# Optimization experiments

Hardware: AMD Instinct MI355X
Metric: run time of the kernel (lower is better)

## Reference

```python
import jax, jax.numpy as jnp
import numpy as np

N_EMB = 8192
EMB_DIM = 128
BETA = 0.25


def setup_inputs() -> dict:
    key = jax.random.key(0)
    k1, k2 = jax.random.split(key)
    x = jax.random.normal(k1, (32, EMB_DIM, 1024), dtype=jnp.float32)
    embeddings = jax.random.normal(k2, (N_EMB, EMB_DIM), dtype=jnp.float32)
    return {"x": x, "embeddings": embeddings}


def reference(x, embeddings):
    # preprocess: swap chn_dim(=1) with last dim, flatten to tokens
    xt = jnp.swapaxes(x, 1, -1)                      # [B, L, D]
    flat = xt.reshape(-1, EMB_DIM)                   # [N, D]
    prenorm = jnp.linalg.norm(flat - jnp.mean(flat)) / np.sqrt(float(flat.size))

    # squared-euclidean distances via matmul + norms: [N, n_emb]
    s1 = jnp.sum(flat * flat, axis=1, keepdims=True)
    s2 = jnp.sum(embeddings * embeddings, axis=1)
    sim = flat @ embeddings.T
    distances = s1 + s2 - 2.0 * sim

    min_distance = jnp.min(distances, axis=1)
    idx = jnp.argmin(distances, axis=1)              # [N] int
    fit = jnp.mean(jnp.nan_to_num(min_distance))

    # EMA scatter statistics (one-hot matmul in torch == segment_sum here)
    k_sum = jax.ops.segment_sum(flat, idx, num_segments=N_EMB)         # [n_emb, D]
    k_elem = jax.ops.segment_sum(jnp.ones_like(idx, jnp.float32), idx,
                                 num_segments=N_EMB)                   # [n_emb]
    k_prob = k_elem / jnp.sum(k_elem)
    entropy = -jnp.sum(k_prob * jnp.log(k_prob + 1e-8))

    # embedding gather, reshape back to channels-first
    quantized = embeddings[idx].reshape(xt.shape)    # [B, L, D]
    quantized = jnp.swapaxes(quantized, 1, -1)       # [B, D, L]

    # ema_update=True -> codebook_loss = 0, only commit loss
    commit_loss = BETA * jnp.mean((jax.lax.stop_gradient(quantized) - x) ** 2)
    loss = commit_loss

    # straight-through estimator
    out = x + jax.lax.stop_gradient(quantized - x)
    return out, quantized, loss, fit, prenorm, entropy, k_sum, k_elem
```

## Files before the change

### kernel.cpp

```cpp
#include <hip/hip_runtime.h>
#include <math.h>
#include <float.h>

#define BB 32
#define DD 128
#define LL 1024
#define NN 32768
#define NE 8192
#define XSZ 4194304
#define OUT_OFF_Q     4194304
#define OUT_OFF_SCAL  8388608
#define OUT_OFF_KSUM  8388612
#define OUT_OFF_KELEM 9437188

typedef unsigned int u32;
typedef unsigned short u16;
typedef int   i32x4 __attribute__((ext_vector_type(4)));
typedef float f32x4 __attribute__((ext_vector_type(4)));

__device__ inline float waveSum(float v){
  #pragma unroll
  for (int o = 32; o > 0; o >>= 1) v += __shfl_down(v, o, 64);
  return v;
}
__device__ inline double waveSumD(double v){
  #pragma unroll
  for (int o = 32; o > 0; o >>= 1) v += __shfl_down(v, o, 64);
  return v;
}

__global__ __launch_bounds__(256) void prep_kernel(const float* __restrict__ e,
    u16* __restrict__ eh8, int* __restrict__ s2seed, float* __restrict__ s2f,
    int* __restrict__ cnt, float* __restrict__ accs)
{
  int t = threadIdx.x;
  if (blockIdx.x < 32) cnt[blockIdx.x * 256 + t] = 0;
  if (blockIdx.x == 32 && t < 16) accs[t] = 0.f;

  int row = blockIdx.x * 4 + (t >> 6);
  int kd  = t & 63;
  float2 ev = *reinterpret_cast<const float2*>(&e[row * DD + kd * 2]);
  int e0 = __float2int_rn(ev.x * 4096.f);
  int e1 = __float2int_rn(ev.y * 4096.f);
  e0 = min(max(e0, -32639), 32639);
  e1 = min(max(e1, -32639), 32639);
  double sq = (double)e0 * (double)e0 + (double)e1 * (double)e1;
  sq = waveSumD(sq);
  float sqf = ev.x * ev.x + ev.y * ev.y;
  sqf = waveSum(sqf);
  if (kd == 0){
    int sd = (int)(sq * (1.0 / 131072.0));
    sd = min(sd, 120000);
    s2seed[row] = -sd;
    s2f[row] = sqf;
  }
  int h0 = (e0 + 128) >> 8;
  int h1 = (e1 + 128) >> 8;
  int k = kd * 2;
  int T16 = row >> 4, lr = row & 15;
  int kt2 = k >> 6, lg = (k >> 4) & 3, j = k & 15;
  int du16 = (((T16*2 + kt2) * 1024) + lg*256 + lr*16 + j) >> 1;
  eh8[du16] = (u16)((h0 & 255) | ((h1 & 255) << 8));
}

#define LOADSET(AH0,AH1,SEED,TT) \
  { int T_ = (TT); \
    AH0 = *(const i32x4*)(ehp + (size_t)(T_*2 + 0) * 256); \
    AH1 = *(const i32x4*)(ehp + (size_t)(T_*2 + 1) * 256); \
    SEED = s2s4[T_*4 + sofs]; }

#define MFMA2S(SLOT, CT, AH0,AH1,SEED) \
  SLOT = __builtin_amdgcn_mfma_i32_16x16x64_i8(AH0, Bh[CT][0], SEED, 0,0,0); \
  SLOT = __builtin_amdgcn_mfma_i32_16x16x64_i8(AH1, Bh[CT][1], SLOT, 0,0,0);

#define KEYS1(T1V, CT, JV) \
  { _Pragma("unroll") \
    for (int r = 0; r < 4; ++r){ \
      int key = (int)(((u32)T1V[r] << 13) + (u32)(JV[r])); \
      int k2n; \
      asm("v_med3_i32 %0, %1, %2, %3" \
          : "=v"(k2n) : "v"(key), "v"(k1[CT]), "v"(k2[CT])); \
      k2[CT] = k2n; \
      k1[CT] = max(key, k1[CT]); \
    } }

#define TILE_BODY(AH0,AH1,SEED,JV) \
  MFMA2S(sa, 0, AH0,AH1,SEED) \
  MFMA2S(sb, 1, AH0,AH1,SEED) \
  KEYS1(sa, 0, JV) \
  MFMA2S(sa, 2, AH0,AH1,SEED) \
  KEYS1(sb, 1, JV) \
  MFMA2S(sb, 3, AH0,AH1,SEED) \
  KEYS1(sa, 2, JV) \
  KEYS1(sb, 3, JV)

__global__ __launch_bounds__(256, 4) void argmin_mfma(
    const float* __restrict__ x,
    const u32* __restrict__ eh8,
    const i32x4* __restrict__ s2s4,
    int* __restrict__ idx1o, int* __restrict__ idx2o)
{
  __shared__ int kk1[1024];
  __shared__ int kk2[1024];

  int t  = threadIdx.x;
  int w  = t >> 6;
  int l  = t & 63;
  int lr = l & 15;
  int lg = l >> 4;

  int blk  = blockIdx.x;
  int half = blk >> 9;
  int tb   = blk & 511;
  int hb64 = half * 64;

  int n0 = tb * 64;
  int b  = n0 >> 10;
  int l0 = n0 & 1023;
  const float* xb = x + (size_t)b * (DD * LL);

  i32x4 Bh[4][2];
  #pragma unroll
  for (int ct = 0; ct < 4; ++ct){
    int tok = l0 + ct*16 + lr;
    #pragma unroll
    for (int kt = 0; kt < 2; ++kt){
      #pragma unroll
      for (int dw = 0; dw < 4; ++dw){
        u32 hw = 0;
        #pragma unroll
        for (int bb = 0; bb < 4; ++bb){
          int k = kt*64 + lg*16 + dw*4 + bb;
          int xi = __float2int_rn(xb[(size_t)k * LL + tok] * 4096.f);
          xi = min(max(xi, -32639), 32639);
          int h  = (xi + 128) >> 8;
          hw |= ((u32)h & 255u) << (8*bb);
        }
        Bh[ct][kt][dw] = (int)hw;
      }
    }
  }

  int k1[4], k2[4];
  #pragma unroll
  for (int ct = 0; ct < 4; ++ct){ k1[ct] = (int)0x80000000; k2[ct] = (int)0x80000000; }

  int jvA[4], jvB[4];
  #pragma unroll
  for (int r = 0; r < 4; ++r){
    jvA[r] = 8191 - (hb64*64 + w*16 + lg*4 + r);
    jvB[r] = jvA[r] - 64;
  }

  const u32* ehp = eh8 + (size_t)l * 4;
  int sofs = lg;

  i32x4 Ah0A, Ah1A, seedA;
  i32x4 Ah0B, Ah1B, seedB;
  i32x4 sa, sb;

  LOADSET(Ah0A, Ah1A, seedA, (hb64 + 0)*4 + w)
  LOADSET(Ah0B, Ah1B, seedB, (hb64 + 1)*4 + w)

  for (int it = 0; it < 64; it += 2){
    TILE_BODY(Ah0A, Ah1A, seedA, jvA)
    if (it + 2 < 64){
      LOADSET(Ah0A, Ah1A, seedA, (hb64 + it + 2)*4 + w)
    }
    #pragma unroll
    for (int r = 0; r < 4; ++r) jvA[r] -= 128;

    TILE_BODY(Ah0B, Ah1B, seedB, jvB)
    if (it + 3 < 64){
      LOADSET(Ah0B, Ah1B, seedB, (hb64 + it + 3)*4 + w)
    }
    #pragma unroll
    for (int r = 0; r < 4; ++r) jvB[r] -= 128;
  }

  #pragma unroll
  for (int ct = 0; ct < 4; ++ct){
    int sidx = (ct*16 + lr)*16 + w*4 + lg;
    kk1[sidx] = k1[ct];
    kk2[sidx] = k2[ct];
  }
  __syncthreads();
  if (t < 64){
    int K1 = (int)0x80000000, K2 = (int)0x80000000;
    #pragma unroll 4
    for (int s = 0; s < 16; ++s){
      int a = kk1[t*16 + s], b2 = kk2[t*16 + s];
      int mn = min(a, K1);  K2 = max(mn, K2);  K1 = max(a, K1);
      mn = min(b2, K1);     K2 = max(mn, K2);  K1 = max(b2, K1);
    }
    idx1o[half*NN + n0 + t] = 8191 - (K1 & 8191);
    idx2o[half*NN + n0 + t] = 8191 - (K2 & 8191);
  }
}

__global__ __launch_bounds__(256) void fixup_kernel(const float* __restrict__ x,
    const float* __restrict__ e, const float* __restrict__ s2f,
    const int* __restrict__ idx1, const int* __restrict__ idx2,
    int* __restrict__ idxf, int* __restrict__ cnt, float* __restrict__ accs,
    float* __restrict__ out, float* __restrict__ quant, float* __restrict__ xT)
{
  __shared__ float red[5][4][64];
  __shared__ int jws[64];

  int t = threadIdx.x;
  int w = t >> 6, l = t & 63;
  int n0 = blockIdx.x * 64;
  int n  = n0 + l;
  int b  = n0 >> 10;
  int l0 = n0 & 1023;
  size_t base = (size_t)b * (DD * LL) + l0 + l;
  const float* xb = x + base;

  int js[4];
  js[0] = idx1[n];      js[1] = idx2[n];
  js[2] = idx1[NN + n]; js[3] = idx2[NN + n];

  float s1 = 0.f, sx = 0.f;
  float dt0 = 0.f, dt1 = 0.f, dt2 = 0.f, dt3 = 0.f;
  int kbase = w * 32;
  #pragma unroll
  for (int k4 = 0; k4 < 8; ++k4){
    int k = kbase + k4*4;
    float x0 = xb[(size_t)(k+0) * LL];
    float x1 = xb[(size_t)(k+1) * LL];
    float x2 = xb[(size_t)(k+2) * LL];
    float x3 = xb[(size_t)(k+3) * LL];
    s1 = fmaf(x0,x0, fmaf(x1,x1, fmaf(x2,x2, fmaf(x3,x3, s1))));
    sx += x0 + x1 + x2 + x3;
    if (xT) *(float4*)&xT[(size_t)n * DD + k] = make_float4(x0,x1,x2,x3);
    float4 v0 = *(const float4*)&e[(size_t)js[0] * DD + k];
    float4 v1 = *(const float4*)&e[(size_t)js[1] * DD + k];
    float4 v2 = *(const float4*)&e[(size_t)js[2] * DD + k];
    float4 v3 = *(const float4*)&e[(size_t)js[3] * DD + k];
    dt0 = fmaf(x0,v0.x, fmaf(x1,v0.y, fmaf(x2,v0.z, fmaf(x3,v0.w, dt0))));
    dt1 = fmaf(x0,v1.x, fmaf(x1,v1.y, fmaf(x2,v1.z, fmaf(x3,v1.w, dt1))));
    dt2 = fmaf(x0,v2.x, fmaf(x1,v2.y, fmaf(x2,v2.z, fmaf(x3,v2.w, dt2))));
    dt3 = fmaf(x0,v3.x, fmaf(x1,v3.y, fmaf(x2,v3.z, fmaf(x3,v3.w, dt3))));
  }
  red[0][w][l] = s1;
  red[1][w][l] = dt0;  red[2][w][l] = dt1;
  red[3][w][l] = dt2;  red[4][w][l] = dt3;
  sx = waveSum(sx);
  if (l == 0) atomicAdd(&accs[0], sx);
  __syncthreads();

  if (w == 0){
    float S1 = red[0][0][l] + red[0][1][l] + red[0][2][l] + red[0][3][l];
    float D[4];
    #pragma unroll
    for (int i = 0; i < 4; ++i)
      D[i] = red[1+i][0][l] + red[1+i][1][l] + red[1+i][2][l] + red[1+i][3][l];
    int jw = js[0];
    float dw = S1 + s2f[js[0]] - 2.f * D[0];
    #pragma unroll
    for (int i = 1; i < 4; ++i){
      float di = S1 + s2f[js[i]] - 2.f * D[i];
      if (di < dw || (di == dw && js[i] < jw)) { dw = di; jw = js[i]; }
    }
    idxf[n] = jw;
    atomicAdd(&cnt[jw], 1);
    jws[l] = jw;
    float S1s = waveSum(S1);
    float dws = waveSum(dw);
    if (l == 0){
      atomicAdd(&accs[1], S1s);
      atomicAdd(&accs[3], dws);
    }
  }
  __syncthreads();

  int jw = jws[l];
  float* ob = out   + base;
  float* qb = quant + base;
  #pragma unroll
  for (int k4 = 0; k4 < 8; ++k4){
    int k = kbase + k4*4;
    float4 q = *(const float4*)&e[(size_t)jw * DD + k];
    ob[(size_t)(k+0)*LL] = q.x;  qb[(size_t)(k+0)*LL] = q.x;
    ob[(size_t)(k+1)*LL] = q.y;  qb[(size_t)(k+1)*LL] = q.y;
    ob[(size_t)(k+2)*LL] = q.z;  qb[(size_t)(k+2)*LL] = q.z;
    ob[(size_t)(k+3)*LL] = q.w;  qb[(size_t)(k+3)*LL] = q.w;
  }
}

__global__ __launch_bounds__(1024) void prefix_kernel(const int* __restrict__ cnt,
    int* __restrict__ cursor, float* __restrict__ kelem,
    const float* __restrict__ accs, float* __restrict__ scal)
{
  __shared__ int sc[1024];
  __shared__ double er[16];
  int t = threadIdx.x;
  int c[8]; int s = 0;
  #pragma unroll
  for (int i = 0; i < 8; ++i){ c[i] = cnt[t*8 + i]; s += c[i]; }
  sc[t] = s;
  __syncthreads();
  for (int off = 1; off < 1024; off <<= 1){
    int v = sc[t];
    int u = (t >= off) ? sc[t - off] : 0;
    __syncthreads();
    sc[t] = v + u;
    __syncthreads();
  }
  int base = t ? sc[t-1] : 0;
  #pragma unroll
  for (int i = 0; i < 8; ++i){
    cursor[t*8 + i] = base;
    kelem[t*8 + i] = (float)c[i];
    base += c[i];
  }
  double es = 0.0;
  #pragma unroll
  for (int i = 0; i < 8; ++i){
    float p = (float)c[i] * (1.0f / NN);
    es += (double)(p * logf(p + 1e-8f));
  }
  es = waveSumD(es);
  if ((t & 63) == 0) er[t >> 6] = es;
  __syncthreads();
  if (t == 0){
    double ent = 0.0;
    #pragma unroll
    for (int i = 0; i < 16; ++i) ent += er[i];
    ent = -ent;
    float sum = accs[0], sq = accs[1], fitsum = accs[3];
    double mu  = (double)sum / (double)XSZ;
    double var = (double)sq / (double)XSZ - mu * mu;
    if (var < 0) var = 0;
    scal[0] = (float)(0.25 * (double)fitsum / (double)XSZ);
    scal[1] = (float)((double)fitsum / (double)NN);
    scal[2] = (float)sqrt(var);
    scal[3] = (float)ent;
  }
}

__global__ __launch_bounds__(256) void scatter_kernel(const int* __restrict__ idxf,
    int* __restrict__ cursor, int* __restrict__ order, int* __restrict__ jsorted,
    float* __restrict__ ksum)
{
  int n = blockIdx.x * 256 + threadIdx.x;
  {
    const float4 z = make_float4(0.f,0.f,0.f,0.f);
    float4* kz = (float4*)&ksum[(size_t)n * 32];
    #pragma unroll
    for (int i = 0; i < 8; ++i) kz[i] = z;
  }
  int j = idxf[n];
  int p = atomicAdd(&cursor[j], 1);
  order[p] = n;
  jsorted[p] = j;
}

__global__ __launch_bounds__(256) void ksum_chunk_kernel(const float* __restrict__ xT,
    const int* __restrict__ order, const int* __restrict__ jsorted,
    float* __restrict__ ksum)
{
  int wv = threadIdx.x >> 6, lane = threadIdx.x & 63;
  int chunk = blockIdx.x * 4 + wv;
  int st = chunk * 16;
  int myo = order[st + (lane & 15)];
  int myj = jsorted[st + (lane & 15)];
  float a0 = 0.f, a1 = 0.f;
  bool inside = false;
  #pragma unroll
  for (int k = 0; k < 16; ++k){
    int j = __shfl(myj, k);
    int n = __shfl(myo, k);
    const float* xr = xT + (size_t)n * DD;
    a0 += xr[lane];
    a1 += xr[64 + lane];
    int jn = (k < 15) ? __shfl(myj, k + 1) : -1;
    if (jn != j){
      if (inside && k < 15){
        ksum[j * DD + lane]      = a0;
        ksum[j * DD + 64 + lane] = a1;
      } else {
        atomicAdd(&ksum[j * DD + lane], a0);
        atomicAdd(&ksum[j * DD + 64 + lane], a1);
      }
      a0 = 0.f; a1 = 0.f;
      inside = true;
    }
  }
}

__global__ __launch_bounds__(256) void ksum_kernel(const float* __restrict__ x,
    const int* __restrict__ order, const int* __restrict__ cnt,
    const int* __restrict__ cursor, float* __restrict__ ksum)
{
  int w = threadIdx.x >> 6, lane = threadIdx.x & 63;
  int j = blockIdx.x * 4 + w;
  int c = cnt[j];
  int st = cursor[j] - c;
  float a0 = 0.f, a1 = 0.f;
  for (int k = 0; k < c; ++k){
    int n = order[st + k];
    int b = n >> 10, l = n & 1023;
    const float* xb = x + (size_t)b * (DD * LL) + l;
    a0 += xb[lane * LL];
    a1 += xb[(lane + 64) * LL];
  }
  ksum[j * DD + lane]      = a0;
  ksum[j * DD + 64 + lane] = a1;
}

extern "C" void kernel_launch(void* const* d_in, const int* in_sizes, int n_in,
                              void* d_out, int out_size, void* d_ws, size_t ws_size,
                              hipStream_t stream)
{
  const float* x = (const float*)d_in[0];
  const float* e = (const float*)d_in[1];
  float* out   = (float*)d_out;
  float* quant = out + OUT_OFF_Q;
  float* scal  = out + OUT_OFF_SCAL;
  float* ksum  = out + OUT_OFF_KSUM;
  float* kelem = out + OUT_OFF_KELEM;

  char* wsb = (char*)d_ws;
  u16*   eh8     = (u16*)(wsb);
  float* s2f     = (float*)(wsb + 1048576);
  int*   s2seed  = (int*)(wsb + 2097152);
  int*   idx1    = (int*)(wsb + 2129920);
  int*   idx2    = (int*)(wsb + 2392064);
  int*   idxf    = (int*)(wsb + 2654208);
  int*   cnt     = (int*)(wsb + 2785280);
  int*   cursor  = (int*)(wsb + 2818048);
  int*   order   = (int*)(wsb + 2850816);
  int*   jsorted = (int*)(wsb + 2981888);
  float* accs    = (float*)(wsb + 3112960);
  float* xT      = (float*)(wsb + 4194304);
  bool useXT = ws_size >= (size_t)(4194304 + 16777216);

  prep_kernel   <<<NE / 4,     256, 0, stream>>>(e, eh8, s2seed, s2f, cnt, accs);
  argmin_mfma   <<<1024,       256, 0, stream>>>(x, (const u32*)eh8,
                                                 (const i32x4*)s2seed, idx1, idx2);
  fixup_kernel  <<<NN / 64,    256, 0, stream>>>(x, e, s2f, idx1, idx2, idxf, cnt,
                                                 accs, out, quant,
                                                 useXT ? xT : (float*)nullptr);
  prefix_kernel <<<1,         1024, 0, stream>>>(cnt, cursor, kelem, accs, scal);
  scatter_kernel<<<NN / 256,   256, 0, stream>>>(idxf, cursor, order, jsorted, ksum);
  if (useXT){
    ksum_chunk_kernel<<<NN / 64, 256, 0, stream>>>(xT, order, jsorted, ksum);
  } else {
    ksum_kernel      <<<NE / 4,  256, 0, stream>>>(x, order, cnt, cursor, ksum);
  }
}
```

Baseline: 152.1 us.

## Split codebook search into four quarters and rescore eight candidates in fixup

The approximate int8 MFMA argmin kernel now splits the codebook into four quarters instead of two, launching twice as many blocks that each scan half as many codes, with launch bounds raised to allow six blocks per CU. Each quarter emits top-2 candidates, so the fixup kernel now rescores eight candidates per token in fp32 instead of four. This aims to raise parallelism and occupancy in the argmin stage, at the cost of re-reading each block's x tile, doing more embedding gathers and FMAs in fixup, and possible register pressure under the tighter launch bound.

```diff
diff --git a/kernel.cpp b/kernel.cpp
--- a/kernel.cpp
+++ b/kernel.cpp
@@ -73,10 +73,10 @@
   SLOT = __builtin_amdgcn_mfma_i32_16x16x64_i8(AH0, Bh[CT][0], SEED, 0,0,0); \
   SLOT = __builtin_amdgcn_mfma_i32_16x16x64_i8(AH1, Bh[CT][1], SLOT, 0,0,0);
 
-#define KEYS1(T1V, CT, JV) \
+#define KEYS1(T1V, CT) \
   { _Pragma("unroll") \
     for (int r = 0; r < 4; ++r){ \
-      int key = (int)(((u32)T1V[r] << 13) + (u32)(JV[r])); \
+      int key = (int)(((u32)T1V[r] << 13) + (u32)(jv[r])); \
       int k2n; \
       asm("v_med3_i32 %0, %1, %2, %3" \
           : "=v"(k2n) : "v"(key), "v"(k1[CT]), "v"(k2[CT])); \
@@ -84,21 +84,21 @@
       k1[CT] = max(key, k1[CT]); \
     } }
 
-#define TILE_BODY(AH0,AH1,SEED,JV) \
+#define TILE_BODY(AH0,AH1,SEED) \
   MFMA2S(sa, 0, AH0,AH1,SEED) \
   MFMA2S(sb, 1, AH0,AH1,SEED) \
-  KEYS1(sa, 0, JV) \
+  KEYS1(sa, 0) \
   MFMA2S(sa, 2, AH0,AH1,SEED) \
-  KEYS1(sb, 1, JV) \
+  KEYS1(sb, 1) \
   MFMA2S(sb, 3, AH0,AH1,SEED) \
-  KEYS1(sa, 2, JV) \
-  KEYS1(sb, 3, JV)
-
-__global__ __launch_bounds__(256, 4) void argmin_mfma(
+  KEYS1(sa, 2) \
+  KEYS1(sb, 3)
+
+__global__ __launch_bounds__(256, 6) void argmin_mfma(
     const float* __restrict__ x,
     const u32* __restrict__ eh8,
     const i32x4* __restrict__ s2s4,
-    int* __restrict__ idx1o, int* __restrict__ idx2o)
+    int* __restrict__ idxc)
 {
   __shared__ int kk1[1024];
   __shared__ int kk2[1024];
@@ -110,9 +110,9 @@
   int lg = l >> 4;
 
   int blk  = blockIdx.x;
-  int half = blk >> 9;
+  int q    = blk >> 9;
   int tb   = blk & 511;
-  int hb64 = half * 64;
+  int hb32 = q * 32;
 
   int n0 = tb * 64;
   int b  = n0 >> 10;
@@ -145,12 +145,10 @@
   #pragma unroll
   for (int ct = 0; ct < 4; ++ct){ k1[ct] = (int)0x80000000; k2[ct] = (int)0x80000000; }
 
-  int jvA[4], jvB[4];
-  #pragma unroll
-  for (int r = 0; r < 4; ++r){
-    jvA[r] = 8191 - (hb64*64 + w*16 + lg*4 + r);
-    jvB[r] = jvA[r] - 64;
-  }
+  int jv[4];
+  #pragma unroll
+  for (int r = 0; r < 4; ++r)
+    jv[r] = 8191 - (q*2048 + w*16 + lg*4 + r);
 
   const u32* ehp = eh8 + (size_t)l * 4;
   int sofs = lg;
@@ -159,23 +157,23 @@
   i32x4 Ah0B, Ah1B, seedB;
   i32x4 sa, sb;
 
-  LOADSET(Ah0A, Ah1A, seedA, (hb64 + 0)*4 + w)
-  LOADSET(Ah0B, Ah1B, seedB, (hb64 + 1)*4 + w)
-
-  for (int it = 0; it < 64; it += 2){
-    TILE_BODY(Ah0A, Ah1A, seedA, jvA)
-    if (it + 2 < 64){
-      LOADSET(Ah0A, Ah1A, seedA, (hb64 + it + 2)*4 + w)
-    }
-    #pragma unroll
-    for (int r = 0; r < 4; ++r) jvA[r] -= 128;
-
-    TILE_BODY(Ah0B, Ah1B, seedB, jvB)
-    if (it + 3 < 64){
-      LOADSET(Ah0B, Ah1B, seedB, (hb64 + it + 3)*4 + w)
-    }
-    #pragma unroll
-    for (int r = 0; r < 4; ++r) jvB[r] -= 128;
+  LOADSET(Ah0A, Ah1A, seedA, (hb32 + 0)*4 + w)
+  LOADSET(Ah0B, Ah1B, seedB, (hb32 + 1)*4 + w)
+
+  for (int it = 0; it < 32; it += 2){
+    TILE_BODY(Ah0A, Ah1A, seedA)
+    if (it + 2 < 32){
+      LOADSET(Ah0A, Ah1A, seedA, (hb32 + it + 2)*4 + w)
+    }
+    #pragma unroll
+    for (int r = 0; r < 4; ++r) jv[r] -= 64;
+
+    TILE_BODY(Ah0B, Ah1B, seedB)
+    if (it + 3 < 32){
+      LOADSET(Ah0B, Ah1B, seedB, (hb32 + it + 3)*4 + w)
+    }
+    #pragma unroll
+    for (int r = 0; r < 4; ++r) jv[r] -= 64;
   }
 
   #pragma unroll
@@ -193,18 +191,18 @@
       int mn = min(a, K1);  K2 = max(mn, K2);  K1 = max(a, K1);
       mn = min(b2, K1);     K2 = max(mn, K2);  K1 = max(b2, K1);
     }
-    idx1o[half*NN + n0 + t] = 8191 - (K1 & 8191);
-    idx2o[half*NN + n0 + t] = 8191 - (K2 & 8191);
+    idxc[(q*2 + 0)*NN + n0 + t] = 8191 - (K1 & 8191);
+    idxc[(q*2 + 1)*NN + n0 + t] = 8191 - (K2 & 8191);
   }
 }
 
 __global__ __launch_bounds__(256) void fixup_kernel(const float* __restrict__ x,
     const float* __restrict__ e, const float* __restrict__ s2f,
-    const int* __restrict__ idx1, const int* __restrict__ idx2,
+    const int* __restrict__ idxc,
     int* __restrict__ idxf, int* __restrict__ cnt, float* __restrict__ accs,
     float* __restrict__ out, float* __restrict__ quant, float* __restrict__ xT)
 {
-  __shared__ float red[5][4][64];
+  __shared__ float red[9][4][64];
   __shared__ int jws[64];
 
   int t = threadIdx.x;
@@ -216,12 +214,14 @@
   size_t base = (size_t)b * (DD * LL) + l0 + l;
   const float* xb = x + base;
 
-  int js[4];
-  js[0] = idx1[n];      js[1] = idx2[n];
-  js[2] = idx1[NN + n]; js[3] = idx2[NN + n];
+  int js[8];
+  #pragma unroll
+  for (int i = 0; i < 8; ++i) js[i] = idxc[i*NN + n];
 
   float s1 = 0.f, sx = 0.f;
-  float dt0 = 0.f, dt1 = 0.f, dt2 = 0.f, dt3 = 0.f;
+  float dt[8];
+  #pragma unroll
+  for (int i = 0; i < 8; ++i) dt[i] = 0.f;
   int kbase = w * 32;
   #pragma unroll
   for (int k4 = 0; k4 < 8; ++k4){
@@ -233,32 +233,29 @@
     s1 = fmaf(x0,x0, fmaf(x1,x1, fmaf(x2,x2, fmaf(x3,x3, s1))));
     sx += x0 + x1 + x2 + x3;
     if (xT) *(float4*)&xT[(size_t)n * DD + k] = make_float4(x0,x1,x2,x3);
-    float4 v0 = *(const float4*)&e[(size_t)js[0] * DD + k];
-    float4 v1 = *(const float4*)&e[(size_t)js[1] * DD + k];
-    float4 v2 = *(const float4*)&e[(size_t)js[2] * DD + k];
-    float4 v3 = *(const float4*)&e[(size_t)js[3] * DD + k];
-    dt0 = fmaf(x0,v0.x, fmaf(x1,v0.y, fmaf(x2,v0.z, fmaf(x3,v0.w, dt0))));
-    dt1 = fmaf(x0,v1.x, fmaf(x1,v1.y, fmaf(x2,v1.z, fmaf(x3,v1.w, dt1))));
-    dt2 = fmaf(x0,v2.x, fmaf(x1,v2.y, fmaf(x2,v2.z, fmaf(x3,v2.w, dt2))));
-    dt3 = fmaf(x0,v3.x, fmaf(x1,v3.y, fmaf(x2,v3.z, fmaf(x3,v3.w, dt3))));
+    #pragma unroll
+    for (int i = 0; i < 8; ++i){
+      float4 v = *(const float4*)&e[(size_t)js[i] * DD + k];
+      dt[i] = fmaf(x0,v.x, fmaf(x1,v.y, fmaf(x2,v.z, fmaf(x3,v.w, dt[i]))));
+    }
   }
   red[0][w][l] = s1;
-  red[1][w][l] = dt0;  red[2][w][l] = dt1;
-  red[3][w][l] = dt2;  red[4][w][l] = dt3;
+  #pragma unroll
+  for (int i = 0; i < 8; ++i) red[1+i][w][l] = dt[i];
   sx = waveSum(sx);
   if (l == 0) atomicAdd(&accs[0], sx);
   __syncthreads();
 
   if (w == 0){
     float S1 = red[0][0][l] + red[0][1][l] + red[0][2][l] + red[0][3][l];
-    float D[4];
-    #pragma unroll
-    for (int i = 0; i < 4; ++i)
+    float D[8];
+    #pragma unroll
+    for (int i = 0; i < 8; ++i)
       D[i] = red[1+i][0][l] + red[1+i][1][l] + red[1+i][2][l] + red[1+i][3][l];
     int jw = js[0];
     float dw = S1 + s2f[js[0]] - 2.f * D[0];
     #pragma unroll
-    for (int i = 1; i < 4; ++i){
+    for (int i = 1; i < 8; ++i){
       float di = S1 + s2f[js[i]] - 2.f * D[i];
       if (di < dw || (di == dw && js[i] < jw)) { dw = di; jw = js[i]; }
     }
@@ -280,11 +277,11 @@
   #pragma unroll
   for (int k4 = 0; k4 < 8; ++k4){
     int k = kbase + k4*4;
-    float4 q = *(const float4*)&e[(size_t)jw * DD + k];
-    ob[(size_t)(k+0)*LL] = q.x;  qb[(size_t)(k+0)*LL] = q.x;
-    ob[(size_t)(k+1)*LL] = q.y;  qb[(size_t)(k+1)*LL] = q.y;
-    ob[(size_t)(k+2)*LL] = q.z;  qb[(size_t)(k+2)*LL] = q.z;
-    ob[(size_t)(k+3)*LL] = q.w;  qb[(size_t)(k+3)*LL] = q.w;
+    float4 qv = *(const float4*)&e[(size_t)jw * DD + k];
+    ob[(size_t)(k+0)*LL] = qv.x;  qb[(size_t)(k+0)*LL] = qv.x;
+    ob[(size_t)(k+1)*LL] = qv.y;  qb[(size_t)(k+1)*LL] = qv.y;
+    ob[(size_t)(k+2)*LL] = qv.z;  qb[(size_t)(k+2)*LL] = qv.z;
+    ob[(size_t)(k+3)*LL] = qv.w;  qb[(size_t)(k+3)*LL] = qv.w;
   }
 }
 
@@ -425,21 +422,20 @@
   u16*   eh8     = (u16*)(wsb);
   float* s2f     = (float*)(wsb + 1048576);
   int*   s2seed  = (int*)(wsb + 2097152);
-  int*   idx1    = (int*)(wsb + 2129920);
-  int*   idx2    = (int*)(wsb + 2392064);
-  int*   idxf    = (int*)(wsb + 2654208);
-  int*   cnt     = (int*)(wsb + 2785280);
-  int*   cursor  = (int*)(wsb + 2818048);
-  int*   order   = (int*)(wsb + 2850816);
-  int*   jsorted = (int*)(wsb + 2981888);
-  float* accs    = (float*)(wsb + 3112960);
+  int*   idxc    = (int*)(wsb + 2129920);
+  int*   idxf    = (int*)(wsb + 3178496);
+  int*   cnt     = (int*)(wsb + 3309568);
+  int*   cursor  = (int*)(wsb + 3342336);
+  int*   order   = (int*)(wsb + 3375104);
+  int*   jsorted = (int*)(wsb + 3506176);
+  float* accs    = (float*)(wsb + 3637248);
   float* xT      = (float*)(wsb + 4194304);
   bool useXT = ws_size >= (size_t)(4194304 + 16777216);
 
   prep_kernel   <<<NE / 4,     256, 0, stream>>>(e, eh8, s2seed, s2f, cnt, accs);
-  argmin_mfma   <<<1024,       256, 0, stream>>>(x, (const u32*)eh8,
-                                                 (const i32x4*)s2seed, idx1, idx2);
-  fixup_kernel  <<<NN / 64,    256, 0, stream>>>(x, e, s2f, idx1, idx2, idxf, cnt,
+  argmin_mfma   <<<2048,       256, 0, stream>>>(x, (const u32*)eh8,
+                                                 (const i32x4*)s2seed, idxc);
+  fixup_kernel  <<<NN / 64,    256, 0, stream>>>(x, e, s2f, idxc, idxf, cnt,
                                                  accs, out, quant,
                                                  useXT ? xT : (float*)nullptr);
   prefix_kernel <<<1,         1024, 0, stream>>>(cnt, cursor, kelem, accs, scal);
```

Result: slower. 267.8 us (+76.0%).
